# Kernel tuning notes

Hardware: AMD Instinct MI355X
Metric: run time of the kernel (lower is better)

## Reference

```python
import jax, jax.numpy as jnp
import numpy as np
from jax import lax
from jax.scipy.special import logsumexp

B, T, C = 512, 512, 64


def setup_inputs() -> dict:
    key = jax.random.key(0)
    k1, k2, k3, k4, k5 = jax.random.split(key, 5)
    emissions = jax.random.normal(k1, (B, T, C), dtype=jnp.float32)
    tags = jax.random.randint(k2, (B, T), 0, C, dtype=jnp.int32)
    mask = jnp.ones((B, T), dtype=jnp.int32)
    transitions = jax.random.normal(k3, (C, C), dtype=jnp.float32)
    start_transitions = jax.random.normal(k4, (C,), dtype=jnp.float32)
    end_transitions = jax.random.normal(k5, (C,), dtype=jnp.float32)
    return {"emissions": emissions, "tags": tags, "mask": mask,
            "transitions": transitions, "start_transitions": start_transitions,
            "end_transitions": end_transitions}


def _log_partition(emissions, maskb, transitions, start_transitions, end_transitions):
    # forward algorithm: lp [B,C] carried over T-1 steps
    lp0 = start_transitions[None, :] + emissions[:, 0]  # [B,C]

    def step(lp, xs):
        emit_t, mask_t = xs  # [B,C], [B]
        # score[b,i,j] = lp[b,i] + trans[i,j] + emit[b,j]
        score = lp[:, :, None] + transitions[None, :, :] + emit_t[:, None, :]
        lp_next = logsumexp(score, axis=1)  # [B,C]
        lp = jnp.where(mask_t[:, None], lp_next, lp)
        return lp, None

    xs = (jnp.swapaxes(emissions[:, 1:], 0, 1), jnp.swapaxes(maskb[:, 1:], 0, 1))
    lp, _ = lax.scan(step, lp0, xs)
    return logsumexp(lp + end_transitions[None, :], axis=1)  # [B]


def _joint_score(emissions, tags, mask, maskb, transitions, start_transitions, end_transitions):
    b_idx = jnp.arange(emissions.shape[0])
    score0 = start_transitions[tags[:, 0]] + emissions[b_idx, 0, tags[:, 0]]  # [B]
    trans = transitions[tags[:, :-1], tags[:, 1:]]  # [B,T-1]
    emit = jnp.take_along_axis(emissions, tags[:, :, None], axis=2)[:, :, 0]  # [B,T]
    step_scores = jnp.where(maskb[:, 1:], trans + emit[:, 1:], 0.0)
    last_idx = jnp.sum(mask, axis=1).astype(jnp.int32) - 1
    last_tags = tags[b_idx, last_idx]
    return score0 + jnp.sum(step_scores, axis=1) + end_transitions[last_tags]


def reference(emissions, tags, mask, transitions, start_transitions, end_transitions):
    maskb = mask.astype(bool)
    log_denominator = _log_partition(emissions, maskb, transitions, start_transitions, end_transitions)
    log_numerator = _joint_score(emissions, tags, mask, maskb, transitions, start_transitions, end_transitions)
    return jnp.mean(log_denominator - log_numerator)
```

## Files before the change

kernel.cpp:

```cpp
#include <hip/hip_runtime.h>

#define Bn 512
#define Tn 512
#define Cn 64


template <int CTRL>
__device__ __forceinline__ float fmax_dpp(const float v) {
    const int o = __builtin_amdgcn_update_dpp(__float_as_int(v), __float_as_int(v),
                                              CTRL, 0xF, 0xF, false);
    return fmaxf(v, __int_as_float(o));
}

__device__ __forceinline__ float wave_max64(float v) {
    v = fmax_dpp<0x0B1>(v);
    v = fmax_dpp<0x04E>(v);
    v = fmax_dpp<0x141>(v);
    v = fmax_dpp<0x140>(v);
    v = fmax_dpp<0x142>(v);
    v = fmax_dpp<0x143>(v);
    return __int_as_float(__builtin_amdgcn_readlane(__float_as_int(v), 63));
}

__global__ __launch_bounds__(64) void crf_half_kernel(
    const float* __restrict__ emissions,
    const int*   __restrict__ tags,
    const int*   __restrict__ mask,
    const float* __restrict__ transitions,
    const float* __restrict__ start_t,
    const float* __restrict__ end_t,
    float*       __restrict__ ws_alpha,
    float*       __restrict__ ws_beta,
    float*       __restrict__ ws_lsF,
    float*       __restrict__ ws_lsB,
    float*       __restrict__ ws_num)
{
    const int  blk = blockIdx.x;
    const bool fwd = blk < Bn;
    const int  bt  = blk & (Bn - 1);
    const int  j   = threadIdx.x;

    const float* em  = emissions + (size_t)bt * Tn * Cn + j;
    const float* em0 = emissions + (size_t)bt * Tn * Cn;
    const int*   mk  = mask + bt * Tn;
    const int*   tg  = tags + bt * Tn;

    if (fwd) {
        float nsum = 0.f;
        int   mcnt = 0;
        for (int t = j; t < Tn; t += 64) {
            const int tag_t = tg[t];
            const int m_t   = mk[t];
            mcnt += m_t;
            if (t >= 1 && m_t) {
                const int tag_p = tg[t - 1];
                nsum += transitions[tag_p * Cn + tag_t] + em0[t * Cn + tag_t];
            }
        }
#pragma unroll
        for (int off = 32; off > 0; off >>= 1) {
            nsum += __shfl_xor(nsum, off, 64);
            mcnt += __shfl_xor(mcnt, off, 64);
        }

        float w[Cn];
#pragma unroll
        for (int i = 0; i < Cn; ++i) w[i] = __expf(transitions[i * Cn + j]);

        float lp0 = start_t[j] + em[0];
        const float m0 = wave_max64(lp0);
        float log_scale = m0;
        float a_self = __expf(lp0 - m0);

        float cur_e[4];
        int   cur_m[4];
#pragma unroll
        for (int k = 0; k < 4; ++k) {
            cur_e[k] = em[(size_t)(1 + k) * Cn];
            cur_m[k] = mk[1 + k];
        }

        for (int g = 0; g < 64; ++g) {
            float nxt_e[4];
            int   nxt_m[4];
#pragma unroll
            for (int k = 0; k < 4; ++k) {
                const int t = 4 * g + 5 + k;
                nxt_e[k] = em[(size_t)t * Cn];
                nxt_m[k] = mk[t];
            }
            float ex[4];
#pragma unroll
            for (int k = 0; k < 4; ++k) ex[k] = __expf(cur_e[k]);

#pragma unroll
            for (int k = 0; k < 4; ++k) {
                float au[Cn];
#pragma unroll
                for (int i = 0; i < Cn; ++i)
                    au[i] = __int_as_float(
                        __builtin_amdgcn_readlane(__float_as_int(a_self), i));

                float acc0 = 0.f, acc1 = 0.f, acc2 = 0.f, acc3 = 0.f;
#pragma unroll
                for (int i = 0; i < Cn; i += 4) {
                    acc0 = fmaf(au[i + 0], w[i + 0], acc0);
                    acc1 = fmaf(au[i + 1], w[i + 1], acc1);
                    acc2 = fmaf(au[i + 2], w[i + 2], acc2);
                    acc3 = fmaf(au[i + 3], w[i + 3], acc3);
                }
                float s = ((acc0 + acc1) + (acc2 + acc3)) * ex[k];
                if (!cur_m[k]) s = a_self;
                if (k == 3) {
                    const float mx = wave_max64(s);
                    s *= __builtin_amdgcn_rcpf(mx);
                    log_scale += __logf(mx);
                }
                a_self = s;
            }
#pragma unroll
            for (int k = 0; k < 4; ++k) {
                cur_e[k] = nxt_e[k];
                cur_m[k] = nxt_m[k];
            }
        }

        ws_alpha[bt * Cn + j] = a_self;
        if (j == 0) {
            ws_lsF[bt] = log_scale;
            const int t0 = tg[0];
            const int tl = tg[mcnt - 1];
            ws_num[bt] = start_t[t0] + em0[t0] + nsum + end_t[tl];
        }
    } else {
        float w[Cn];
#pragma unroll
        for (int i = 0; i < Cn; ++i) w[i] = __expf(transitions[j * Cn + i]);

        float lp0 = end_t[j];
        const float m0 = wave_max64(lp0);
        float log_scale = m0;
        float b_self = __expf(lp0 - m0);

        float cur_e[4];
        int   cur_m[4];
#pragma unroll
        for (int k = 0; k < 4; ++k) {
            const int u = Tn - 1 - k;
            cur_e[k] = em[(size_t)u * Cn];
            cur_m[k] = mk[u];
        }

        for (int g = 0; g < 64; ++g) {
            float nxt_e[4];
            int   nxt_m[4];
#pragma unroll
            for (int k = 0; k < 4; ++k) {
                const int u = Tn - 5 - 4 * g - k;
                nxt_e[k] = em[(size_t)u * Cn];
                nxt_m[k] = mk[u];
            }
            float ex[4];
#pragma unroll
            for (int k = 0; k < 4; ++k) ex[k] = __expf(cur_e[k]);

#pragma unroll
            for (int k = 0; k < 4; ++k) {
                const int s_idx = 4 * g + k;
                if (s_idx < Tn / 2 - 1) {
                    const float wv = b_self * ex[k];
                    float au[Cn];
#pragma unroll
                    for (int i = 0; i < Cn; ++i)
                        au[i] = __int_as_float(
                            __builtin_amdgcn_readlane(__float_as_int(wv), i));

                    float acc0 = 0.f, acc1 = 0.f, acc2 = 0.f, acc3 = 0.f;
#pragma unroll
                    for (int i = 0; i < Cn; i += 4) {
                        acc0 = fmaf(au[i + 0], w[i + 0], acc0);
                        acc1 = fmaf(au[i + 1], w[i + 1], acc1);
                        acc2 = fmaf(au[i + 2], w[i + 2], acc2);
                        acc3 = fmaf(au[i + 3], w[i + 3], acc3);
                    }
                    float s = ((acc0 + acc1) + (acc2 + acc3));
                    if (!cur_m[k]) s = b_self;
                    if (k == 3) {
                        const float mx = wave_max64(s);
                        s *= __builtin_amdgcn_rcpf(mx);
                        log_scale += __logf(mx);
                    }
                    b_self = s;
                }
            }
#pragma unroll
            for (int k = 0; k < 4; ++k) {
                cur_e[k] = nxt_e[k];
                cur_m[k] = nxt_m[k];
            }
        }

        ws_beta[bt * Cn + j] = b_self;
        if (j == 0) ws_lsB[bt] = log_scale;
    }
}

__global__ __launch_bounds__(64) void crf_combine_kernel(
    const float* __restrict__ ws_alpha,
    const float* __restrict__ ws_beta,
    const float* __restrict__ ws_lsF,
    const float* __restrict__ ws_lsB,
    const float* __restrict__ ws_num,
    float*       __restrict__ out)
{
    const int bt = blockIdx.x;
    const int j  = threadIdx.x;
    float v = ws_alpha[bt * Cn + j] * ws_beta[bt * Cn + j];
#pragma unroll
    for (int off = 32; off > 0; off >>= 1) v += __shfl_xor(v, off, 64);
    if (j == 0) {
        const float denom = ws_lsF[bt] + ws_lsB[bt] + __logf(v);
        atomicAdd(out, (denom - ws_num[bt]) * (1.0f / Bn));
    }
}

__global__ void crf_zero_kernel(float* out) { out[0] = 0.f; }

extern "C" void kernel_launch(void* const* d_in, const int* in_sizes, int n_in,
                              void* d_out, int out_size, void* d_ws, size_t ws_size,
                              hipStream_t stream)
{
    const float* emissions   = (const float*)d_in[0];
    const int*   tags        = (const int*)d_in[1];
    const int*   mask        = (const int*)d_in[2];
    const float* transitions = (const float*)d_in[3];
    const float* start_t     = (const float*)d_in[4];
    const float* end_t       = (const float*)d_in[5];

    float* ws       = (float*)d_ws;
    float* ws_alpha = ws;
    float* ws_beta  = ws_alpha + Bn * Cn;
    float* ws_lsF   = ws_beta + Bn * Cn;
    float* ws_lsB   = ws_lsF + Bn;
    float* ws_num   = ws_lsB + Bn;

    crf_zero_kernel<<<1, 1, 0, stream>>>((float*)d_out);
    crf_half_kernel<<<2 * Bn, Cn, 0, stream>>>(emissions, tags, mask, transitions,
                                               start_t, end_t,
                                               ws_alpha, ws_beta, ws_lsF, ws_lsB, ws_num);
    crf_combine_kernel<<<Bn, Cn, 0, stream>>>(ws_alpha, ws_beta, ws_lsF, ws_lsB,
                                              ws_num, (float*)d_out);
}
```

Before: 173.0 us.

## Broadcast via ds_bpermute, defer rescale, pin weights, batch combine reduction

```diff
diff --git a/kernel.cpp b/kernel.cpp
--- a/kernel.cpp
+++ b/kernel.cpp
@@ -22,7 +22,24 @@
     return __int_as_float(__builtin_amdgcn_readlane(__float_as_int(v), 63));
 }
 
-__global__ __launch_bounds__(64) void crf_half_kernel(
+__device__ __forceinline__ float bcast_dot64(const float a, const float* __restrict__ w) {
+    const int ai = __float_as_int(a);
+    float acc0 = 0.f, acc1 = 0.f, acc2 = 0.f, acc3 = 0.f;
+#pragma unroll
+    for (int i = 0; i < Cn; i += 4) {
+        const float b0 = __int_as_float(__builtin_amdgcn_ds_bpermute(4 * (i + 0), ai));
+        const float b1 = __int_as_float(__builtin_amdgcn_ds_bpermute(4 * (i + 1), ai));
+        const float b2 = __int_as_float(__builtin_amdgcn_ds_bpermute(4 * (i + 2), ai));
+        const float b3 = __int_as_float(__builtin_amdgcn_ds_bpermute(4 * (i + 3), ai));
+        acc0 = fmaf(b0, w[i + 0], acc0);
+        acc1 = fmaf(b1, w[i + 1], acc1);
+        acc2 = fmaf(b2, w[i + 2], acc2);
+        acc3 = fmaf(b3, w[i + 3], acc3);
+    }
+    return (acc0 + acc1) + (acc2 + acc3);
+}
+
+__global__ __launch_bounds__(64, 1) void crf_half_kernel(
     const float* __restrict__ emissions,
     const int*   __restrict__ tags,
     const int*   __restrict__ mask,
@@ -66,11 +83,14 @@
         float w[Cn];
 #pragma unroll
         for (int i = 0; i < Cn; ++i) w[i] = __expf(transitions[i * Cn + j]);
+#pragma unroll
+        for (int i = 0; i < Cn; ++i) asm volatile("" : "+v"(w[i]));
 
         float lp0 = start_t[j] + em[0];
         const float m0 = wave_max64(lp0);
         float log_scale = m0;
         float a_self = __expf(lp0 - m0);
+        float c_pend = 1.0f;
 
         float cur_e[4];
         int   cur_m[4];
@@ -95,25 +115,15 @@
 
 #pragma unroll
             for (int k = 0; k < 4; ++k) {
-                float au[Cn];
-#pragma unroll
-                for (int i = 0; i < Cn; ++i)
-                    au[i] = __int_as_float(
-                        __builtin_amdgcn_readlane(__float_as_int(a_self), i));
-
-                float acc0 = 0.f, acc1 = 0.f, acc2 = 0.f, acc3 = 0.f;
-#pragma unroll
-                for (int i = 0; i < Cn; i += 4) {
-                    acc0 = fmaf(au[i + 0], w[i + 0], acc0);
-                    acc1 = fmaf(au[i + 1], w[i + 1], acc1);
-                    acc2 = fmaf(au[i + 2], w[i + 2], acc2);
-                    acc3 = fmaf(au[i + 3], w[i + 3], acc3);
+                float s = bcast_dot64(a_self, w) * ex[k];
+                if (!cur_m[k]) s = a_self;
+                if (k == 0) {
+                    s *= c_pend;
+                    c_pend = 1.0f;
                 }
-                float s = ((acc0 + acc1) + (acc2 + acc3)) * ex[k];
-                if (!cur_m[k]) s = a_self;
                 if (k == 3) {
                     const float mx = wave_max64(s);
-                    s *= __builtin_amdgcn_rcpf(mx);
+                    c_pend = __builtin_amdgcn_rcpf(mx);
                     log_scale += __logf(mx);
                 }
                 a_self = s;
@@ -125,6 +135,7 @@
             }
         }
 
+        a_self *= c_pend;
         ws_alpha[bt * Cn + j] = a_self;
         if (j == 0) {
             ws_lsF[bt] = log_scale;
@@ -136,11 +147,14 @@
         float w[Cn];
 #pragma unroll
         for (int i = 0; i < Cn; ++i) w[i] = __expf(transitions[j * Cn + i]);
+#pragma unroll
+        for (int i = 0; i < Cn; ++i) asm volatile("" : "+v"(w[i]));
 
         float lp0 = end_t[j];
         const float m0 = wave_max64(lp0);
         float log_scale = m0;
         float b_self = __expf(lp0 - m0);
+        float c_pend = 1.0f;
 
         float cur_e[4];
         int   cur_m[4];
@@ -168,26 +182,16 @@
             for (int k = 0; k < 4; ++k) {
                 const int s_idx = 4 * g + k;
                 if (s_idx < Tn / 2 - 1) {
-                    const float wv = b_self * ex[k];
-                    float au[Cn];
-#pragma unroll
-                    for (int i = 0; i < Cn; ++i)
-                        au[i] = __int_as_float(
-                            __builtin_amdgcn_readlane(__float_as_int(wv), i));
-
-                    float acc0 = 0.f, acc1 = 0.f, acc2 = 0.f, acc3 = 0.f;
-#pragma unroll
-                    for (int i = 0; i < Cn; i += 4) {
-                        acc0 = fmaf(au[i + 0], w[i + 0], acc0);
-                        acc1 = fmaf(au[i + 1], w[i + 1], acc1);
-                        acc2 = fmaf(au[i + 2], w[i + 2], acc2);
-                        acc3 = fmaf(au[i + 3], w[i + 3], acc3);
+                    const float wval = b_self * ex[k];
+                    float s = bcast_dot64(wval, w);
+                    if (!cur_m[k]) s = b_self;
+                    if (k == 0) {
+                        s *= c_pend;
+                        c_pend = 1.0f;
                     }
-                    float s = ((acc0 + acc1) + (acc2 + acc3));
-                    if (!cur_m[k]) s = b_self;
                     if (k == 3) {
                         const float mx = wave_max64(s);
-                        s *= __builtin_amdgcn_rcpf(mx);
+                        c_pend = __builtin_amdgcn_rcpf(mx);
                         log_scale += __logf(mx);
                     }
                     b_self = s;
@@ -200,12 +204,13 @@
             }
         }
 
+        b_self *= c_pend;
         ws_beta[bt * Cn + j] = b_self;
         if (j == 0) ws_lsB[bt] = log_scale;
     }
 }
 
-__global__ __launch_bounds__(64) void crf_combine_kernel(
+__global__ __launch_bounds__(1024) void crf_combine_kernel(
     const float* __restrict__ ws_alpha,
     const float* __restrict__ ws_beta,
     const float* __restrict__ ws_lsF,
@@ -213,14 +218,24 @@
     const float* __restrict__ ws_num,
     float*       __restrict__ out)
 {
-    const int bt = blockIdx.x;
-    const int j  = threadIdx.x;
+    const int wv = threadIdx.x >> 6;
+    const int j  = threadIdx.x & 63;
+    const int bt = blockIdx.x * 16 + wv;
+
+    __shared__ float part[16];
+
     float v = ws_alpha[bt * Cn + j] * ws_beta[bt * Cn + j];
 #pragma unroll
     for (int off = 32; off > 0; off >>= 1) v += __shfl_xor(v, off, 64);
     if (j == 0) {
-        const float denom = ws_lsF[bt] + ws_lsB[bt] + __logf(v);
-        atomicAdd(out, (denom - ws_num[bt]) * (1.0f / Bn));
+        part[wv] = ws_lsF[bt] + ws_lsB[bt] + __logf(v) - ws_num[bt];
+    }
+    __syncthreads();
+    if (threadIdx.x < 64) {
+        float p = (j < 16) ? part[j] : 0.f;
+#pragma unroll
+        for (int off = 32; off > 0; off >>= 1) p += __shfl_xor(p, off, 64);
+        if (j == 0) atomicAdd(out, p * (1.0f / Bn));
     }
 }
 
@@ -248,6 +263,6 @@
     crf_half_kernel<<<2 * Bn, Cn, 0, stream>>>(emissions, tags, mask, transitions,
                                                start_t, end_t,
                                                ws_alpha, ws_beta, ws_lsF, ws_lsB, ws_num);
-    crf_combine_kernel<<<Bn, Cn, 0, stream>>>(ws_alpha, ws_beta, ws_lsF, ws_lsB,
-                                              ws_num, (float*)d_out);
-}
+    crf_combine_kernel<<<Bn / 16, 1024, 0, stream>>>(ws_alpha, ws_beta, ws_lsF, ws_lsB,
+                                                     ws_num, (float*)d_out);
+}
```

Measured after the change: 171.3 us. About the same (-1.0%).
